# Kernel tuning notes

Hardware: AMD Instinct MI355X
Metric: run time of the kernel (lower is better)

Reference implementation:

```python
import jax, jax.numpy as jnp
import numpy as np

N0, N1, N2, N3, N4 = 50000, 100000, 20000, 20000, 20000
E0, E1, E01 = 800000, 1600000, 200000
C = 64
SLOPE = 0.2


def _xavier(k, shape):
    fan_in, fan_out = shape[0], shape[-1]
    lim = float(np.sqrt(6.0 / (fan_in + fan_out)))
    return jax.random.uniform(k, shape, minval=-lim, maxval=lim, dtype=jnp.float32)


def setup_inputs() -> dict:
    key = jax.random.key(0)
    ks = jax.random.split(key, 16)
    return {
        "x_0": jax.random.normal(ks[0], (N0, C), jnp.float32),
        "x_1": jax.random.normal(ks[1], (N1, C), jnp.float32),
        "x_2": jax.random.normal(ks[2], (N2, C), jnp.float32),
        "x_3": jax.random.normal(ks[3], (N3, C), jnp.float32),
        "x_4": jax.random.normal(ks[4], (N4, C), jnp.float32),
        # sparse adjacency_0 [N0,N0], adjacency_1 [N1,N1] as COO (row=i target, col=j source), values=1
        "adj0_idx": jax.random.randint(ks[5], (2, E0), 0, N0, dtype=jnp.int32),
        "adj1_idx": jax.random.randint(ks[6], (2, E1), 0, N1, dtype=jnp.int32),
        # sparse incidence_0_1 [N0,N1]: row = 0-cell (target), col = 1-cell (source)
        "inc01_t": jax.random.randint(ks[7], (E01,), 0, N0, dtype=jnp.int32),
        "inc01_s": jax.random.randint(ks[8], (E01,), 0, N1, dtype=jnp.int32),
        # HBS_0 params
        "W0": _xavier(ks[9], (C, C)),
        "a0": _xavier(ks[10], (2 * C, 1))[:, 0],
        # HBS_1 params
        "W1": _xavier(ks[11], (C, C)),
        "a1": _xavier(ks[12], (2 * C, 1))[:, 0],
        # HBNS params (source = x_1, target = x_0)
        "Ws": _xavier(ks[13], (C, C)),
        "Wt": _xavier(ks[14], (C, C)),
        "a_ns": _xavier(ks[15], (2 * C, 1))[:, 0],
    }


def _row_norm(vals, rows, n_rows):
    # sparse row-sum normalization (softmax_attention=False path)
    rs = jax.ops.segment_sum(vals, rows, num_segments=n_rows)
    denom = jnp.where(rs == 0, 1.0, rs)
    return vals / denom[rows]


def _hbs(x, idx, W, a, n):
    # Higher-order attention Block for Squared neighborhoods, m_hop=1.
    m = x @ W                               # [n, C]
    i, j = idx[0], idx[1]                   # edge (i <- j)
    # score_ij = leaky_relu(cat(m_i, m_j) @ a) computed without materializing [E, 2C]
    p_l = m @ a[:C]                         # [n]
    p_r = m @ a[C:]                         # [n]
    e = jax.nn.leaky_relu(p_l[i] + p_r[j], SLOPE)   # [E]
    att = _row_norm(e, i, n)                # [E]
    # (att .* A) @ m  with binary A values
    return jax.ops.segment_sum(att[:, None] * m[j], i, num_segments=n)


def _hbns(x_s, x_t, t_idx, s_idx, Ws, Wt, a, n_s, n_t):
    # Higher-order attention Block for Non-Squared neighborhoods.
    sm = x_s @ Ws                           # [n_s, C] messages from source cells
    tm = x_t @ Wt                           # [n_t, C] messages from target cells
    p_s = sm @ a[:C]                        # [n_s]
    p_t = tm @ a[C:]                        # [n_t]
    e = jax.nn.leaky_relu(p_s[s_idx] + p_t[t_idx], SLOPE)   # [E01]
    att_s_to_t = _row_norm(e, t_idx, n_t)   # normalize per target row
    att_t_to_s = _row_norm(e, s_idx, n_s)   # normalize per source row (transposed)
    msg_on_target = jax.ops.segment_sum(att_s_to_t[:, None] * sm[s_idx], t_idx, num_segments=n_t)
    msg_on_source = jax.ops.segment_sum(att_t_to_s[:, None] * tm[t_idx], s_idx, num_segments=n_s)
    return msg_on_source, msg_on_target    # (x_0_to_1, x_1_to_0)


def reference(x_0, x_1, x_2, x_3, x_4, adj0_idx, adj1_idx, inc01_t, inc01_s,
              W0, a0, W1, a1, Ws, Wt, a_ns):
    x_0_to_0 = _hbs(x_0, adj0_idx, W0, a0, N0)
    x_1_to_1 = _hbs(x_1, adj1_idx, W1, a1, N1)
    x_0_to_1, x_1_to_0 = _hbns(x_1, x_0, inc01_t, inc01_s, Ws, Wt, a_ns, N1, N0)
    # Aggregation(aggr_func='sum', update_func=None)
    x_0_level1 = x_0_to_0 + x_1_to_0
    x_1_level1 = x_1_to_1 + x_0_to_1
    return (x_0_level1, x_1_level1, x_2, x_3, x_4)
```

## Files before the change

### kernel.cpp

```cpp
#include <hip/hip_runtime.h>

#define CDIM 64
#define SLOPE 0.2f
#define PART_EDGES 8192
#define BW 128

__device__ __forceinline__ float lrelu(float v) { return v > 0.f ? v : SLOPE * v; }

struct PartDesc {
    const int* keys[4];
    const int* vals[4];
    int E[4];
    int nb[4];
    int bcap[4];
    int bufbase[4];
    int pblk[5];
};

struct FrontDesc {
    PartDesc pd;
    const float *X0, *W0, *Wt, *a0;
    float *m0, *tm, *pl0, *pr0, *plt, *prt;
    int n0, t0;
    const float *X1, *W1, *Ws, *a1, *ans;
    float *m1, *sm, *pl1, *pr1, *pls, *prs;
    int n1, t1;
    const float4 *c0, *c1, *c2;
    float4* dst;
    int n4;
};

__device__ void partition_body(const PartDesc& d, int b, int2* __restrict__ gbuf,
                               int* __restrict__ bcur, int* hist, int* sbase)
{
    int l = (b >= d.pblk[2]) ? ((b >= d.pblk[3]) ? 3 : 2) : ((b >= d.pblk[1]) ? 1 : 0);
    const int start = (b - d.pblk[l]) * PART_EDGES;
    const int E = d.E[l];
    const int nb = d.nb[l];
    const int t = threadIdx.x;
    for (int i = t; i < nb; i += 256) hist[i] = 0;
    __syncthreads();
    const int* kp = d.keys[l];
    const int* vp = d.vals[l];

#pragma unroll
    for (int seg = 0; seg < 8; ++seg) {
        int i4 = start + seg * 1024 + t * 4;
        if (i4 + 3 < E) {
            int4 k4 = *reinterpret_cast<const int4*>(kp + i4);
            atomicAdd(&hist[k4.x >> 7], 1);
            atomicAdd(&hist[k4.y >> 7], 1);
            atomicAdd(&hist[k4.z >> 7], 1);
            atomicAdd(&hist[k4.w >> 7], 1);
        } else {
            int e4 = min(i4 + 4, E);
            for (int u = i4; u < e4; ++u) atomicAdd(&hist[kp[u] >> 7], 1);
        }
    }
    __syncthreads();
    for (int i = t; i < nb; i += 256) {
        int c = hist[i];
        sbase[i] = c ? atomicAdd(&bcur[l * 1024 + i], c) : 0;
    }
    __syncthreads();
    for (int i = t; i < nb; i += 256) hist[i] = 0;
    __syncthreads();

    const int bcap = d.bcap[l];
    int2* buf = gbuf + d.bufbase[l];
#pragma unroll
    for (int seg = 0; seg < 8; ++seg) {
        int i4 = start + seg * 1024 + t * 4;
        if (i4 + 3 < E) {
            int4 k4 = *reinterpret_cast<const int4*>(kp + i4);
            int4 v4 = *reinterpret_cast<const int4*>(vp + i4);
            int ks[4] = { k4.x, k4.y, k4.z, k4.w };
            int vs[4] = { v4.x, v4.y, v4.z, v4.w };
#pragma unroll
            for (int e = 0; e < 4; ++e) {
                int bk = ks[e] >> 7;
                int r = atomicAdd(&hist[bk], 1);
                int slot = sbase[bk] + r;
                if (slot < bcap) buf[(size_t)bk * bcap + slot] = make_int2(ks[e], vs[e]);
            }
        } else {
            int e4 = min(i4 + 4, E);
            for (int u = i4; u < e4; ++u) {
                int k = kp[u];
                int bk = k >> 7;
                int r = atomicAdd(&hist[bk], 1);
                int slot = sbase[bk] + r;
                if (slot < bcap) buf[(size_t)bk * bcap + slot] = make_int2(k, vp[u]);
            }
        }
    }
}

__device__ void gemm_tile_p(const float* __restrict__ X,
                            const float* __restrict__ Wa, float* __restrict__ Ya,
                            const float* __restrict__ aa, float* __restrict__ pLa, float* __restrict__ pRa,
                            const float* __restrict__ Wb, float* __restrict__ Yb,
                            const float* __restrict__ ab, float* __restrict__ pLb, float* __restrict__ pRb,
                            int n, int tile,
                            float* sX, float* sWaT, float* sWbT, float* sa2)
{
    const int tid = threadIdx.x;
    const int lane = tid & 63;
    const int q = tid >> 6;

    for (int idx = tid; idx < 4096; idx += 256) {
        int k = idx >> 6, c = idx & 63;
        sWaT[c * 66 + k] = Wa[idx];
        sWbT[c * 66 + k] = Wb[idx];
    }
    if (tid < 128) sa2[tid] = aa[tid];
    else sa2[tid] = ab[tid - 128];

    const int rowbase = tile << 6;
#pragma unroll
    for (int i = 0; i < 4; ++i) {
        int f = tid + i * 256;
        int r = f >> 4, k4 = f & 15;
        int row = rowbase + r;
        float4 v = make_float4(0.f, 0.f, 0.f, 0.f);
        if (row < n) v = *reinterpret_cast<const float4*>(X + (size_t)row * 64 + k4 * 4);
        *reinterpret_cast<float4*>(&sX[r * 68 + k4 * 4]) = v;
    }
    __syncthreads();

    const int r0 = q * 16;
    float accA[16], accB[16];
#pragma unroll
    for (int r = 0; r < 16; ++r) { accA[r] = 0.f; accB[r] = 0.f; }

    for (int k4 = 0; k4 < 16; ++k4) {
        const float2 wa0 = *reinterpret_cast<const float2*>(&sWaT[lane * 66 + k4 * 4]);
        const float2 wa1 = *reinterpret_cast<const float2*>(&sWaT[lane * 66 + k4 * 4 + 2]);
        const float2 wb0 = *reinterpret_cast<const float2*>(&sWbT[lane * 66 + k4 * 4]);
        const float2 wb1 = *reinterpret_cast<const float2*>(&sWbT[lane * 66 + k4 * 4 + 2]);
#pragma unroll
        for (int r = 0; r < 16; ++r) {
            const float4 xv = *reinterpret_cast<const float4*>(&sX[(r0 + r) * 68 + k4 * 4]);
            accA[r] = fmaf(xv.x, wa0.x, accA[r]);
            accA[r] = fmaf(xv.y, wa0.y, accA[r]);
            accA[r] = fmaf(xv.z, wa1.x, accA[r]);
            accA[r] = fmaf(xv.w, wa1.y, accA[r]);
            accB[r] = fmaf(xv.x, wb0.x, accB[r]);
            accB[r] = fmaf(xv.y, wb0.y, accB[r]);
            accB[r] = fmaf(xv.z, wb1.x, accB[r]);
            accB[r] = fmaf(xv.w, wb1.y, accB[r]);
        }
    }
#pragma unroll
    for (int r = 0; r < 16; ++r) {
        int row = rowbase + r0 + r;
        if (row < n) {
            Ya[(size_t)row * 64 + lane] = accA[r];
            Yb[(size_t)row * 64 + lane] = accB[r];
        }
    }

    __syncthreads();
#pragma unroll
    for (int r = 0; r < 16; ++r) sX[(r0 + r) * 68 + lane] = accA[r];
    __syncthreads();
    if (tid < 64) {
        int row = rowbase + tid;
        if (row < n) {
            const float4* rp = reinterpret_cast<const float4*>(&sX[tid * 68]);
            float sl = 0.f, sr = 0.f;
#pragma unroll
            for (int k4 = 0; k4 < 16; ++k4) {
                float4 xv = rp[k4];
                float4 al = *reinterpret_cast<const float4*>(&sa2[k4 * 4]);
                float4 ar = *reinterpret_cast<const float4*>(&sa2[64 + k4 * 4]);
                sl = fmaf(xv.x, al.x, sl); sl = fmaf(xv.y, al.y, sl);
                sl = fmaf(xv.z, al.z, sl); sl = fmaf(xv.w, al.w, sl);
                sr = fmaf(xv.x, ar.x, sr); sr = fmaf(xv.y, ar.y, sr);
                sr = fmaf(xv.z, ar.z, sr); sr = fmaf(xv.w, ar.w, sr);
            }
            pLa[row] = sl;
            pRa[row] = sr;
        }
    }
    __syncthreads();
#pragma unroll
    for (int r = 0; r < 16; ++r) sX[(r0 + r) * 68 + lane] = accB[r];
    __syncthreads();
    if (tid < 64) {
        int row = rowbase + tid;
        if (row < n) {
            const float4* rp = reinterpret_cast<const float4*>(&sX[tid * 68]);
            float sl = 0.f, sr = 0.f;
#pragma unroll
            for (int k4 = 0; k4 < 16; ++k4) {
                float4 xv = rp[k4];
                float4 al = *reinterpret_cast<const float4*>(&sa2[128 + k4 * 4]);
                float4 ar = *reinterpret_cast<const float4*>(&sa2[192 + k4 * 4]);
                sl = fmaf(xv.x, al.x, sl); sl = fmaf(xv.y, al.y, sl);
                sl = fmaf(xv.z, al.z, sl); sl = fmaf(xv.w, al.w, sl);
                sr = fmaf(xv.x, ar.x, sr); sr = fmaf(xv.y, ar.y, sr);
                sr = fmaf(xv.z, ar.z, sr); sr = fmaf(xv.w, ar.w, sr);
            }
            pLb[row] = sl;
            pRb[row] = sr;
        }
    }
}

__global__ __launch_bounds__(256) void front_kernel(FrontDesc fd, int2* __restrict__ gbuf,
                                                    int* __restrict__ bcur)
{
    __shared__ float sX[64 * 68];
    __shared__ float sWaT[64 * 66];
    __shared__ float sWbT[64 * 66];
    __shared__ float sa2[256];

    int b = blockIdx.x;
    const int nPart = fd.pd.pblk[4];
    if (b < nPart) {
        partition_body(fd.pd, b, gbuf, bcur, (int*)sX, ((int*)sX) + 1024);
        return;
    }
    b -= nPart;
    if (b < fd.t0) {
        gemm_tile_p(fd.X0, fd.W0, fd.m0, fd.a0, fd.pl0, fd.pr0,
                    fd.Wt, fd.tm, fd.ans, fd.plt, fd.prt,
                    fd.n0, b, sX, sWaT, sWbT, sa2);
        return;
    }
    b -= fd.t0;
    if (b < fd.t1) {
        gemm_tile_p(fd.X1, fd.W1, fd.m1, fd.a1, fd.pl1, fd.pr1,
                    fd.Ws, fd.sm, fd.ans, fd.pls, fd.prs,
                    fd.n1, b, sX, sWaT, sWbT, sa2);
        return;
    }
    b -= fd.t1;
    int i = b * 256 + threadIdx.x;
    int n4 = fd.n4;
    if (i < n4)            fd.dst[i] = fd.c0[i];
    else if (i < 2 * n4)   fd.dst[i] = fd.c1[i - n4];
    else if (i < 3 * n4)   fd.dst[i] = fd.c2[i - 2 * n4];
}

struct GB {
    const int2* bufA; const int* curA; int bcapA;
    const float* MA; const float* plA; const float* prA;
    const int2* bufB; const int* curB; int bcapB;
    const float* MB; const float* plB; const float* prB;
    float* out; int n;
};

__device__ __forceinline__ void gatherrow_lds(const int* __restrict__ sorted, int s0, int deg,
                                              const float* __restrict__ M,
                                              const float* __restrict__ pr,
                                              float pl, int gg, int c4,
                                              float4& acc, double& se)
{
    for (int p = 0; p < deg; p += 8) {
        int i1 = p + gg;
        int i2 = p + 4 + gg;
        bool ok1 = i1 < deg;
        bool ok2 = i2 < deg;
        int j1 = ok1 ? sorted[s0 + i1] : 0;
        int j2 = ok2 ? sorted[s0 + i2] : 0;
        float e1 = ok1 ? lrelu(pl + pr[j1]) : 0.f;
        float e2 = ok2 ? lrelu(pl + pr[j2]) : 0.f;
        const float4 r1 = *reinterpret_cast<const float4*>(M + (size_t)j1 * 64 + c4);
        const float4 r2 = *reinterpret_cast<const float4*>(M + (size_t)j2 * 64 + c4);
        se += (double)e1 + (double)e2;
        acc.x = fmaf(e1, r1.x, fmaf(e2, r2.x, acc.x));
        acc.y = fmaf(e1, r1.y, fmaf(e2, r2.y, acc.y));
        acc.z = fmaf(e1, r1.z, fmaf(e2, r2.z, acc.z));
        acc.w = fmaf(e1, r1.w, fmaf(e2, r2.w, acc.w));
    }
}

__global__ __launch_bounds__(512) void gatherbkt_kernel(GB ga, GB gb, int nbSplit)
{
    __shared__ int countsA[BW], startsA[BW], cursA[BW];
    __shared__ int countsB[BW], startsB[BW], cursB[BW];
    __shared__ int sortedA[2560];
    __shared__ int sortedB[768];

    const bool first = blockIdx.x < nbSplit;
    GB g = first ? ga : gb;
    const int bucket = first ? blockIdx.x : (blockIdx.x - nbSplit);
    const int lo = bucket * BW;
    const int t = threadIdx.x;

    if (t < BW) { countsA[t] = 0; countsB[t] = 0; }
    __syncthreads();

    const int cntA = min(g.curA[bucket], g.bcapA);
    const int cntB = min(g.curB[bucket], g.bcapB);
    const int2* bufA = g.bufA + (size_t)bucket * g.bcapA;
    const int2* bufB = g.bufB + (size_t)bucket * g.bcapB;

    for (int i = t; i < cntA; i += 512) atomicAdd(&countsA[bufA[i].x - lo], 1);
    for (int i = t; i < cntB; i += 512) atomicAdd(&countsB[bufB[i].x - lo], 1);
    __syncthreads();

    {
        int idx = t & (BW - 1);
        bool a = t < BW;
        bool b = (t >= BW) && (t < 2 * BW);
        if (a) startsA[idx] = countsA[idx];
        if (b) startsB[idx] = countsB[idx];
        __syncthreads();
        for (int off = 1; off < BW; off <<= 1) {
            int vA = (a && idx >= off) ? startsA[idx - off] : 0;
            int vB = (b && idx >= off) ? startsB[idx - off] : 0;
            __syncthreads();
            if (a) startsA[idx] += vA;
            if (b) startsB[idx] += vB;
            __syncthreads();
        }
        if (a) { startsA[idx] -= countsA[idx]; cursA[idx] = startsA[idx]; }
        if (b) { startsB[idx] -= countsB[idx]; cursB[idx] = startsB[idx]; }
    }
    __syncthreads();
    for (int i = t; i < cntA; i += 512) {
        int2 kv = bufA[i];
        sortedA[atomicAdd(&cursA[kv.x - lo], 1)] = kv.y;
    }
    for (int i = t; i < cntB; i += 512) {
        int2 kv = bufB[i];
        sortedB[atomicAdd(&cursB[kv.x - lo], 1)] = kv.y;
    }
    __syncthreads();

    const int lane = t & 63;
    const int wid = t >> 6;
    const int gg = lane >> 4;
    const int c4 = (lane & 15) << 2;

    for (int rr = wid; rr < BW; rr += 8) {
        int row = lo + rr;
        if (row >= g.n) break;
        float4 accA = make_float4(0.f, 0.f, 0.f, 0.f);
        float4 accB = make_float4(0.f, 0.f, 0.f, 0.f);
        double seA = 0.0, seB = 0.0;

        gatherrow_lds(sortedA, startsA[rr], countsA[rr], g.MA, g.prA, g.plA[row], gg, c4, accA, seA);
        gatherrow_lds(sortedB, startsB[rr], countsB[rr], g.MB, g.prB, g.plB[row], gg, c4, accB, seB);

        seA += __shfl_xor(seA, 16, 64); seA += __shfl_xor(seA, 32, 64);
        seB += __shfl_xor(seB, 16, 64); seB += __shfl_xor(seB, 32, 64);
        float rA = (float)(1.0 / ((seA == 0.0) ? 1.0 : seA));
        float rB = (float)(1.0 / ((seB == 0.0) ? 1.0 : seB));

        float4 part;
        part.x = accA.x * rA + accB.x * rB;
        part.y = accA.y * rA + accB.y * rB;
        part.z = accA.z * rA + accB.z * rB;
        part.w = accA.w * rA + accB.w * rB;
        part.x += __shfl_xor(part.x, 16, 64); part.x += __shfl_xor(part.x, 32, 64);
        part.y += __shfl_xor(part.y, 16, 64); part.y += __shfl_xor(part.y, 32, 64);
        part.z += __shfl_xor(part.z, 16, 64); part.z += __shfl_xor(part.z, 32, 64);
        part.w += __shfl_xor(part.w, 16, 64); part.w += __shfl_xor(part.w, 32, 64);

        if (gg == 0) *reinterpret_cast<float4*>(g.out + (size_t)row * 64 + c4) = part;
    }
}

extern "C" void kernel_launch(void* const* d_in, const int* in_sizes, int n_in,
                              void* d_out, int out_size, void* d_ws, size_t ws_size,
                              hipStream_t stream)
{
    const float* x0  = (const float*)d_in[0];
    const float* x1  = (const float*)d_in[1];
    const float* x2  = (const float*)d_in[2];
    const float* x3  = (const float*)d_in[3];
    const float* x4  = (const float*)d_in[4];
    const int*   adj0 = (const int*)d_in[5];
    const int*   adj1 = (const int*)d_in[6];
    const int*   inct = (const int*)d_in[7];
    const int*   incs = (const int*)d_in[8];
    const float* W0  = (const float*)d_in[9];
    const float* a0  = (const float*)d_in[10];
    const float* W1  = (const float*)d_in[11];
    const float* a1  = (const float*)d_in[12];
    const float* Ws  = (const float*)d_in[13];
    const float* Wt  = (const float*)d_in[14];
    const float* ans = (const float*)d_in[15];

    const int N0  = in_sizes[0] / CDIM;
    const int N1  = in_sizes[1] / CDIM;
    const int NP  = in_sizes[2];
    const int E0  = in_sizes[5] / 2;
    const int E1  = in_sizes[6] / 2;
    const int E01 = in_sizes[7];

    float* out0 = (float*)d_out;
    float* out1 = out0 + (size_t)N0 * CDIM;
    float* outp = out1 + (size_t)N1 * CDIM;

    char* w = (char*)d_ws;
    size_t off = 0;
    float* m0  = (float*)(w + off); off += (size_t)N0 * CDIM * 4;
    float* m1  = (float*)(w + off); off += (size_t)N1 * CDIM * 4;
    float* sm  = (float*)(w + off); off += (size_t)N1 * CDIM * 4;
    float* tm  = (float*)(w + off); off += (size_t)N0 * CDIM * 4;
    float* pl0 = (float*)(w + off); off += (size_t)N0 * 4;
    float* pr0 = (float*)(w + off); off += (size_t)N0 * 4;
    float* pl1 = (float*)(w + off); off += (size_t)N1 * 4;
    float* pr1 = (float*)(w + off); off += (size_t)N1 * 4;
    float* pls = (float*)(w + off); off += (size_t)N1 * 4;
    float* prs = (float*)(w + off); off += (size_t)N1 * 4;
    float* plt = (float*)(w + off); off += (size_t)N0 * 4;
    float* prt = (float*)(w + off); off += (size_t)N0 * 4;
    int* bcur = (int*)(w + off); off += 4096 * 4;
    const int nb0 = (N0 + BW - 1) / BW;
    const int nb1 = (N1 + BW - 1) / BW;
    const int BC0 = 2560, BC1 = 2560, BCT = 768, BCS = 512;
    int2* gbuf = (int2*)(w + off);
    (void)ws_size; (void)n_in; (void)out_size;

    FrontDesc fd;
    PartDesc& d = fd.pd;
    d.keys[0] = adj0; d.vals[0] = adj0 + E0; d.E[0] = E0;  d.nb[0] = nb0; d.bcap[0] = BC0;
    d.keys[1] = adj1; d.vals[1] = adj1 + E1; d.E[1] = E1;  d.nb[1] = nb1; d.bcap[1] = BC1;
    d.keys[2] = inct; d.vals[2] = incs;      d.E[2] = E01; d.nb[2] = nb0; d.bcap[2] = BCT;
    d.keys[3] = incs; d.vals[3] = inct;      d.E[3] = E01; d.nb[3] = nb1; d.bcap[3] = BCS;
    d.bufbase[0] = 0;
    d.bufbase[1] = d.bufbase[0] + nb0 * BC0;
    d.bufbase[2] = d.bufbase[1] + nb1 * BC1;
    d.bufbase[3] = d.bufbase[2] + nb0 * BCT;
    d.pblk[0] = 0;
    for (int l = 0; l < 4; ++l) d.pblk[l + 1] = d.pblk[l] + (d.E[l] + PART_EDGES - 1) / PART_EDGES;

    fd.X0 = x0; fd.W0 = W0; fd.Wt = Wt; fd.a0 = a0;
    fd.m0 = m0; fd.tm = tm; fd.pl0 = pl0; fd.pr0 = pr0; fd.plt = plt; fd.prt = prt;
    fd.n0 = N0; fd.t0 = (N0 + 63) / 64;
    fd.X1 = x1; fd.W1 = W1; fd.Ws = Ws; fd.a1 = a1; fd.ans = ans;
    fd.m1 = m1; fd.sm = sm; fd.pl1 = pl1; fd.pr1 = pr1; fd.pls = pls; fd.prs = prs;
    fd.n1 = N1; fd.t1 = (N1 + 63) / 64;
    fd.c0 = (const float4*)x2; fd.c1 = (const float4*)x3; fd.c2 = (const float4*)x4;
    fd.dst = (float4*)outp; fd.n4 = NP / 4;

    const int nCopyBlk = (3 * fd.n4 + 255) / 256;
    const int nFront = d.pblk[4] + fd.t0 + fd.t1 + nCopyBlk;

    hipMemsetAsync(bcur, 0, 4096 * 4, stream);
    front_kernel<<<nFront, 256, 0, stream>>>(fd, gbuf, bcur);

    GB gb0 = { gbuf + d.bufbase[0], bcur + 0 * 1024, BC0, m0, pl0, pr0,
               gbuf + d.bufbase[2], bcur + 2 * 1024, BCT, sm, prt, pls,
               out0, N0 };
    GB gb1 = { gbuf + d.bufbase[1], bcur + 1 * 1024, BC1, m1, pl1, pr1,
               gbuf + d.bufbase[3], bcur + 3 * 1024, BCS, tm, pls, prt,
               out1, N1 };
    gatherbkt_kernel<<<nb0 + nb1, 512, 0, stream>>>(gb0, gb1, nb0);
}
```

Baseline: 255.6 us.

## Move passthrough copy into gather kernel and merge attention-score passes

The copy of x_2..x_4 into the output moves from the front kernel into extra trailing blocks of the gather kernel, so it can fill idle CUs during the gather tail. Inside the GEMM tile, both accumulator sets are staged to LDS at once (the second into the weight buffer, which is now free). Two thread groups then compute the left and right scores concurrently, removing one round of barriers. The gather kernel's copy blocks reserve its large static LDS even though they do not use it, which can limit how many copy blocks run at once.

```diff
diff --git a/kernel.cpp b/kernel.cpp
--- a/kernel.cpp
+++ b/kernel.cpp
@@ -25,9 +25,6 @@
     const float *X1, *W1, *Ws, *a1, *ans;
     float *m1, *sm, *pl1, *pr1, *pls, *prs;
     int n1, t1;
-    const float4 *c0, *c1, *c2;
-    float4* dst;
-    int n4;
 };
 
 __device__ void partition_body(const PartDesc& d, int b, int2* __restrict__ gbuf,
@@ -162,7 +159,10 @@
 
     __syncthreads();
 #pragma unroll
-    for (int r = 0; r < 16; ++r) sX[(r0 + r) * 68 + lane] = accA[r];
+    for (int r = 0; r < 16; ++r) {
+        sX[(r0 + r) * 68 + lane] = accA[r];
+        sWbT[(r0 + r) * 66 + lane] = accB[r];
+    }
     __syncthreads();
     if (tid < 64) {
         int row = rowbase + tid;
@@ -182,25 +182,22 @@
             pLa[row] = sl;
             pRa[row] = sr;
         }
-    }
-    __syncthreads();
-#pragma unroll
-    for (int r = 0; r < 16; ++r) sX[(r0 + r) * 68 + lane] = accB[r];
-    __syncthreads();
-    if (tid < 64) {
-        int row = rowbase + tid;
+    } else if (tid < 128) {
+        int rl = tid - 64;
+        int row = rowbase + rl;
         if (row < n) {
-            const float4* rp = reinterpret_cast<const float4*>(&sX[tid * 68]);
+            const float2* rp2 = reinterpret_cast<const float2*>(&sWbT[rl * 66]);
             float sl = 0.f, sr = 0.f;
 #pragma unroll
             for (int k4 = 0; k4 < 16; ++k4) {
-                float4 xv = rp[k4];
+                float2 x0 = rp2[k4 * 2 + 0];
+                float2 x1 = rp2[k4 * 2 + 1];
                 float4 al = *reinterpret_cast<const float4*>(&sa2[128 + k4 * 4]);
                 float4 ar = *reinterpret_cast<const float4*>(&sa2[192 + k4 * 4]);
-                sl = fmaf(xv.x, al.x, sl); sl = fmaf(xv.y, al.y, sl);
-                sl = fmaf(xv.z, al.z, sl); sl = fmaf(xv.w, al.w, sl);
-                sr = fmaf(xv.x, ar.x, sr); sr = fmaf(xv.y, ar.y, sr);
-                sr = fmaf(xv.z, ar.z, sr); sr = fmaf(xv.w, ar.w, sr);
+                sl = fmaf(x0.x, al.x, sl); sl = fmaf(x0.y, al.y, sl);
+                sl = fmaf(x1.x, al.z, sl); sl = fmaf(x1.y, al.w, sl);
+                sr = fmaf(x0.x, ar.x, sr); sr = fmaf(x0.y, ar.y, sr);
+                sr = fmaf(x1.x, ar.z, sr); sr = fmaf(x1.y, ar.w, sr);
             }
             pLb[row] = sl;
             pRb[row] = sr;
@@ -230,18 +227,9 @@
         return;
     }
     b -= fd.t0;
-    if (b < fd.t1) {
-        gemm_tile_p(fd.X1, fd.W1, fd.m1, fd.a1, fd.pl1, fd.pr1,
-                    fd.Ws, fd.sm, fd.ans, fd.pls, fd.prs,
-                    fd.n1, b, sX, sWaT, sWbT, sa2);
-        return;
-    }
-    b -= fd.t1;
-    int i = b * 256 + threadIdx.x;
-    int n4 = fd.n4;
-    if (i < n4)            fd.dst[i] = fd.c0[i];
-    else if (i < 2 * n4)   fd.dst[i] = fd.c1[i - n4];
-    else if (i < 3 * n4)   fd.dst[i] = fd.c2[i - 2 * n4];
+    gemm_tile_p(fd.X1, fd.W1, fd.m1, fd.a1, fd.pl1, fd.pr1,
+                fd.Ws, fd.sm, fd.ans, fd.pls, fd.prs,
+                fd.n1, b, sX, sWaT, sWbT, sa2);
 }
 
 struct GB {
@@ -251,6 +239,8 @@
     const float* MB; const float* plB; const float* prB;
     float* out; int n;
 };
+
+struct CopyD { const float4 *c0, *c1, *c2; float4* dst; int n4; };
 
 __device__ __forceinline__ void gatherrow_lds(const int* __restrict__ sorted, int s0, int deg,
                                               const float* __restrict__ M,
@@ -277,12 +267,22 @@
     }
 }
 
-__global__ __launch_bounds__(512) void gatherbkt_kernel(GB ga, GB gb, int nbSplit)
+__global__ __launch_bounds__(512) void gatherbkt_kernel(GB ga, GB gb, int nbSplit,
+                                                        int nbGather, CopyD cd)
 {
     __shared__ int countsA[BW], startsA[BW], cursA[BW];
     __shared__ int countsB[BW], startsB[BW], cursB[BW];
     __shared__ int sortedA[2560];
     __shared__ int sortedB[768];
+
+    if (blockIdx.x >= nbGather) {
+        int i = (blockIdx.x - nbGather) * 512 + threadIdx.x;
+        int n4 = cd.n4;
+        if (i < n4)            cd.dst[i] = cd.c0[i];
+        else if (i < 2 * n4)   cd.dst[i] = cd.c1[i - n4];
+        else if (i < 3 * n4)   cd.dst[i] = cd.c2[i - 2 * n4];
+        return;
+    }
 
     const bool first = blockIdx.x < nbSplit;
     GB g = first ? ga : gb;
@@ -437,11 +437,8 @@
     fd.X1 = x1; fd.W1 = W1; fd.Ws = Ws; fd.a1 = a1; fd.ans = ans;
     fd.m1 = m1; fd.sm = sm; fd.pl1 = pl1; fd.pr1 = pr1; fd.pls = pls; fd.prs = prs;
     fd.n1 = N1; fd.t1 = (N1 + 63) / 64;
-    fd.c0 = (const float4*)x2; fd.c1 = (const float4*)x3; fd.c2 = (const float4*)x4;
-    fd.dst = (float4*)outp; fd.n4 = NP / 4;
-
-    const int nCopyBlk = (3 * fd.n4 + 255) / 256;
-    const int nFront = d.pblk[4] + fd.t0 + fd.t1 + nCopyBlk;
+
+    const int nFront = d.pblk[4] + fd.t0 + fd.t1;
 
     hipMemsetAsync(bcur, 0, 4096 * 4, stream);
     front_kernel<<<nFront, 256, 0, stream>>>(fd, gbuf, bcur);
@@ -452,5 +449,9 @@
     GB gb1 = { gbuf + d.bufbase[1], bcur + 1 * 1024, BC1, m1, pl1, pr1,
                gbuf + d.bufbase[3], bcur + 3 * 1024, BCS, tm, pls, prt,
                out1, N1 };
-    gatherbkt_kernel<<<nb0 + nb1, 512, 0, stream>>>(gb0, gb1, nb0);
-}
+    CopyD cd = { (const float4*)x2, (const float4*)x3, (const float4*)x4,
+                 (float4*)outp, NP / 4 };
+    const int nbGather = nb0 + nb1;
+    const int nCopy = (3 * cd.n4 + 511) / 512;
+    gatherbkt_kernel<<<nbGather + nCopy, 512, 0, stream>>>(gb0, gb1, nb0, nbGather, cd);
+}
```

Measured after the change: 247.5 us. 1.03x faster.
